# Performance work log

Measured on AMD Instinct MI355X. Metric: run time of the kernel, lower is better.

The kernel has to match this reference:

```python
import jax, jax.numpy as jnp
import numpy as np

B, WS, I, H, M_FRAC, PRE = 512, 128, 256, 512, 0.5, 24
NWS = int(WS * M_FRAC)  # 64


def setup_inputs() -> dict:
    key = jax.random.key(0)
    ks = jax.random.split(key, 9)
    s = 0.05
    return {
        "x": jax.random.normal(ks[0], (B, WS, I), dtype=jnp.float32),
        "fc1_w": jax.random.normal(ks[1], (NWS, WS), dtype=jnp.float32) * s,
        "fc1_b": jax.random.normal(ks[2], (NWS,), dtype=jnp.float32) * s,
        "W_ih": jax.random.normal(ks[3], (3 * H, I), dtype=jnp.float32) * s,
        "W_hh": jax.random.normal(ks[4], (3 * H, H), dtype=jnp.float32) * s,
        "b_ih": jax.random.normal(ks[5], (3 * H,), dtype=jnp.float32) * s,
        "b_hh": jax.random.normal(ks[6], (3 * H,), dtype=jnp.float32) * s,
        "fc2_w": jax.random.normal(ks[7], (I, H), dtype=jnp.float32) * s,
        "fc2_b": jax.random.normal(ks[8], (I,), dtype=jnp.float32) * s,
        "pre_len": PRE,
    }


def reference(x, fc1_w, fc1_b, W_ih, W_hh, b_ih, b_hh, fc2_w, fc2_b, pre_len):
    h_dim = W_hh.shape[1]
    # fc1 over the time axis: [B,WS,I] -> transpose -> [B,I,WS] -> [B,I,NWS] -> [B,NWS,I]
    y = jnp.einsum("bit,nt->bin", x.transpose(0, 2, 1), fc1_w) + fc1_b
    y = y.transpose(0, 2, 1)  # [B, NWS, I]

    # Precompute input-side gate projections for all timesteps (one big GEMM)
    gx_all = jnp.einsum("bti,gi->btg", y, W_ih) + b_ih  # [B, NWS, 3H]
    gx_all = gx_all.swapaxes(0, 1)  # time-major [NWS, B, 3H]

    h0 = jnp.zeros((y.shape[0], h_dim), dtype=x.dtype)

    def step(h, gx):
        gh = h @ W_hh.T + b_hh  # [B, 3H]
        r = jax.nn.sigmoid(gx[:, :h_dim] + gh[:, :h_dim])
        z = jax.nn.sigmoid(gx[:, h_dim:2 * h_dim] + gh[:, h_dim:2 * h_dim])
        n = jnp.tanh(gx[:, 2 * h_dim:] + r * gh[:, 2 * h_dim:])
        h_new = (1.0 - z) * n + z * h
        return h_new, h_new

    _, h_seq = jax.lax.scan(step, h0, gx_all)  # [NWS, B, H]
    h_seq = h_seq.swapaxes(0, 1)  # [B, NWS, H]
    out = jnp.einsum("bth,oh->bto", h_seq, fc2_w) + fc2_b  # [B, NWS, I]
    return out[:, -pre_len:, :]
```

## Files before the change

### kernel.cpp

```cpp
#include <hip/hip_runtime.h>
#include <math.h>

#define B_DIM 512
#define WS_DIM 128
#define I_DIM 256
#define H_DIM 512
#define NWS 64
#define PRE 24
#define SEQ0 (NWS - PRE)

typedef __attribute__((ext_vector_type(8))) short short8;
typedef __attribute__((ext_vector_type(4))) float f32x4;

#define MFMA16(a, b, c) __builtin_amdgcn_mfma_f32_16x16x32_bf16((a), (b), (c), 0, 0, 0)

__device__ __forceinline__ unsigned short f2bf(float f) {
    unsigned u = __float_as_uint(f);
    u += 0x7FFF + ((u >> 16) & 1);
    return (unsigned short)(u >> 16);
}
__device__ __forceinline__ float bf2f(unsigned short h) {
    return __uint_as_float(((unsigned)h) << 16);
}

__device__ __forceinline__ unsigned ld_dev(const unsigned* p) {
    return __hip_atomic_load((unsigned*)p, __ATOMIC_RELAXED, __HIP_MEMORY_SCOPE_AGENT);
}
__device__ __forceinline__ unsigned long long ld_dev64(const unsigned long long* p) {
    return __hip_atomic_load((unsigned long long*)p, __ATOMIC_RELAXED, __HIP_MEMORY_SCOPE_AGENT);
}
__device__ __forceinline__ void st_dev(unsigned* p, unsigned v) {
    __hip_atomic_store(p, v, __ATOMIC_RELAXED, __HIP_MEMORY_SCOPE_AGENT);
}

__global__ void __launch_bounds__(256) fc1_kernel(const float* __restrict__ x,
                                                  const float* __restrict__ fc1_w,
                                                  const float* __restrict__ fc1_b,
                                                  unsigned short* __restrict__ y) {
    __shared__ float wsm[NWS * WS_DIM];
    const int b = blockIdx.x;
    const int i = threadIdx.x;

    for (int idx = i; idx < NWS * WS_DIM; idx += 256) wsm[idx] = fc1_w[idx];
    __syncthreads();

    float acc[NWS];
#pragma unroll
    for (int n = 0; n < NWS; ++n) acc[n] = fc1_b[n];

    const float* xb = x + (size_t)b * WS_DIM * I_DIM + i;
    for (int t = 0; t < WS_DIM; ++t) {
        float xv = xb[(size_t)t * I_DIM];
#pragma unroll
        for (int n = 0; n < NWS; ++n) acc[n] += xv * wsm[n * WS_DIM + t];
    }

    unsigned short* yb = y + (size_t)b * NWS * I_DIM + i;
#pragma unroll
    for (int n = 0; n < NWS; ++n) yb[(size_t)n * I_DIM] = f2bf(acc[n]);
}

#define LDSB (24 * 96 * 64)

__global__ void __launch_bounds__(256, 1)
gru_persist(const unsigned short* __restrict__ y,
            const float* __restrict__ Wih, const float* __restrict__ bih,
            const float* __restrict__ Whh, const float* __restrict__ bhh,
            unsigned short* __restrict__ hA,
            unsigned short* __restrict__ hB,
            unsigned short* __restrict__ hseq,
            unsigned* __restrict__ flags) {
    extern __shared__ char lds[];
    const int tid = threadIdx.x;
    const int lane = tid & 63;
    const int w = tid >> 6;
    const int wm = w & 1;
    const int jh = w >> 1;
    const int bt = blockIdx.x & 15;
    const int jt = blockIdx.x >> 4;
    const int b0 = bt * 32;
    const int j0 = jt * 32;

    for (int idx = tid; idx < 96 * 768; idx += 256) {
        int n = idx / 768, k = idx % 768;
        int g = n >> 5, jj = n & 31;
        int srow = g * H_DIM + j0 + jj;
        float wv = (k < I_DIM) ? Wih[(size_t)srow * I_DIM + k]
                               : Whh[(size_t)srow * H_DIM + (k - I_DIM)];
        int ks = k >> 5, q = (k & 31) >> 3, e = k & 7;
        int byteoff = ks * 6144 + (((n * 64 + q * 16) ^ ((n & 7) << 4)) + e * 2);
        *(unsigned short*)(lds + byteoff) = f2bf(wv);
    }

    const int row16 = lane & 15;
    const int qg = lane >> 4;
    const int bbA = b0 + wm * 16 + row16;
    const int jj = jh * 16 + row16;
    const int j = j0 + jj;

    const int n0r = jj, n1r = 32 + jj, n2r = 64 + jj;
    const int bof0 = (n0r * 64 + qg * 16) ^ ((n0r & 7) << 4);
    const int bof1 = (n1r * 64 + qg * 16) ^ ((n1r & 7) << 4);
    const int bof2 = (n2r * 64 + qg * 16) ^ ((n2r & 7) << 4);

    const float br_i = bih[j], br_h = bhh[j];
    const float bz_i = bih[H_DIM + j], bz_h = bhh[H_DIM + j];
    const float bn_i = bih[2 * H_DIM + j], bn_h = bhh[2 * H_DIM + j];

    __syncthreads();

    const unsigned short* ybase = y + (size_t)bbA * NWS * I_DIM + qg * 8;

    short8 yf0[8], yf1[8];
#pragma unroll
    for (int ks = 0; ks < 8; ++ks) yf0[ks] = *(const short8*)(ybase + ks * 32);

    auto STEP = [&](int step, short8(&yc)[8], short8(&yn)[8]) {
        const unsigned short* hin = (step & 1) ? hB : hA;
        unsigned short* hout      = (step & 1) ? hA : hB;

        f32x4 aR = {br_i, br_i, br_i, br_i};
        f32x4 aZ = {bz_i, bz_i, bz_i, bz_i};
        f32x4 aN = {bn_i, bn_i, bn_i, bn_i};

#pragma unroll
        for (int ks = 0; ks < 8; ++ks) {
            short8 bf0 = *(const short8*)(lds + ks * 6144 + bof0);
            short8 bf1 = *(const short8*)(lds + ks * 6144 + bof1);
            short8 bf2 = *(const short8*)(lds + ks * 6144 + bof2);
            aR = MFMA16(yc[ks], bf0, aR);
            aZ = MFMA16(yc[ks], bf1, aZ);
            aN = MFMA16(yc[ks], bf2, aN);
        }

        int sn = (step + 1 < NWS) ? step + 1 : NWS - 1;
        const unsigned short* ypn = ybase + (size_t)sn * I_DIM;
#pragma unroll
        for (int ks = 0; ks < 8; ++ks) yn[ks] = *(const short8*)(ypn + ks * 32);

        if (step > 0) {
            const unsigned* dw = flags + ((size_t)bt * NWS + (step - 1)) * 16;
            while (true) {
                unsigned v = ld_dev(dw + (lane & 15));
                if (__all(v != 0)) break;
                __builtin_amdgcn_s_sleep(1);
            }
            asm volatile("" ::: "memory");
            __syncthreads();
        }

        const unsigned long long* hq = (const unsigned long long*)(hin + (size_t)bbA * H_DIM);
        short8 hf[16];
#pragma unroll
        for (int ks = 0; ks < 16; ++ks) {
            union { unsigned long long u[2]; short8 s; } t;
            t.u[0] = ld_dev64(hq + ks * 8 + qg * 2);
            t.u[1] = ld_dev64(hq + ks * 8 + qg * 2 + 1);
            hf[ks] = t.s;
        }
        unsigned hw[4];
        const unsigned* h32 = (const unsigned*)hin;
#pragma unroll
        for (int r = 0; r < 4; ++r) {
            int brow = b0 + wm * 16 + qg * 4 + r;
            hw[r] = ld_dev(h32 + brow * (H_DIM / 2) + (j >> 1));
        }

        f32x4 hR = {br_h, br_h, br_h, br_h};
        f32x4 hZ = {bz_h, bz_h, bz_h, bz_h};
        f32x4 hN = {bn_h, bn_h, bn_h, bn_h};
#pragma unroll
        for (int ks = 0; ks < 16; ++ks) {
            short8 bf0 = *(const short8*)(lds + (8 + ks) * 6144 + bof0);
            short8 bf1 = *(const short8*)(lds + (8 + ks) * 6144 + bof1);
            short8 bf2 = *(const short8*)(lds + (8 + ks) * 6144 + bof2);
            hR = MFMA16(hf[ks], bf0, hR);
            hZ = MFMA16(hf[ks], bf1, hZ);
            hN = MFMA16(hf[ks], bf2, hN);
        }

        unsigned short hbf[4];
#pragma unroll
        for (int r = 0; r < 4; ++r) {
            int brow = b0 + wm * 16 + qg * 4 + r;
            float pr = aR[r] + hR[r];
            float pz = aZ[r] + hZ[r];
            float rr = 1.f / (1.f + __expf(-pr));
            float zz = 1.f / (1.f + __expf(-pz));
            float pn = aN[r] + rr * hN[r];
            float ax = fabsf(pn);
            float e2 = __expf(2.f * ax);
            float nn = copysignf(1.f - 2.f / (e2 + 1.f), pn);
            float hprev = bf2f((unsigned short)((j & 1) ? (hw[r] >> 16) : (hw[r] & 0xffff)));
            float hnew = (1.f - zz) * nn + zz * hprev;
            hbf[r] = f2bf(hnew);
            unsigned v = hbf[r];
            unsigned o = __shfl_xor(v, 1);
            if (!(lane & 1))
                st_dev((unsigned*)hout + brow * (H_DIM / 2) + (j >> 1), v | (o << 16));
        }

        asm volatile("s_waitcnt vmcnt(0)" ::: "memory");
        __syncthreads();
        if (tid == 0) {
            __hip_atomic_fetch_add(flags + ((size_t)bt * NWS + step) * 16 + jt, 1u,
                                   __ATOMIC_RELAXED, __HIP_MEMORY_SCOPE_AGENT);
        }

        if (step >= SEQ0) {
#pragma unroll
            for (int r = 0; r < 4; ++r) {
                int brow = b0 + wm * 16 + qg * 4 + r;
                unsigned v = hbf[r];
                unsigned o = __shfl_xor(v, 1);
                if (!(lane & 1))
                    *(unsigned*)(hseq + ((size_t)brow * PRE + (step - SEQ0)) * H_DIM +
                                 (j & ~1)) = v | (o << 16);
            }
        }
    };

    for (int step = 0; step < NWS; step += 2) {
        STEP(step, yf0, yf1);
        STEP(step + 1, yf1, yf0);
    }
}

__global__ void __launch_bounds__(256)
fc2_mfma(const unsigned short* __restrict__ hseq,
         const unsigned short* __restrict__ w2,
         const float* __restrict__ bias,
         float* __restrict__ out) {
    const int tid = threadIdx.x;
    const int lane = tid & 63;
    const int w = tid >> 6;
    const int wm = w & 1, wn = w >> 1;
    const int row16 = lane & 15, qg = lane >> 4;
    const int mbase = blockIdx.x * 64 + wm * 32;
    const int nbase = wn * 128;

    f32x4 acc[2][8];
#pragma unroll
    for (int mt = 0; mt < 2; ++mt)
#pragma unroll
        for (int nt = 0; nt < 8; ++nt) acc[mt][nt] = f32x4{0.f, 0.f, 0.f, 0.f};

    const unsigned short* ap = hseq + (size_t)(mbase + row16) * H_DIM + qg * 8;
    const unsigned short* bp = w2 + (size_t)(nbase + row16) * H_DIM + qg * 8;
#pragma unroll
    for (int ks = 0; ks < 16; ++ks) {
        short8 a0 = *(const short8*)(ap + ks * 32);
        short8 a1 = *(const short8*)(ap + 16 * H_DIM + ks * 32);
        short8 bfr[8];
#pragma unroll
        for (int nt = 0; nt < 8; ++nt)
            bfr[nt] = *(const short8*)(bp + (size_t)nt * 16 * H_DIM + ks * 32);
#pragma unroll
        for (int nt = 0; nt < 8; ++nt) {
            acc[0][nt] = MFMA16(a0, bfr[nt], acc[0][nt]);
            acc[1][nt] = MFMA16(a1, bfr[nt], acc[1][nt]);
        }
    }

#pragma unroll
    for (int mt = 0; mt < 2; ++mt)
#pragma unroll
        for (int nt = 0; nt < 8; ++nt)
#pragma unroll
            for (int r = 0; r < 4; ++r) {
                int row = mbase + mt * 16 + qg * 4 + r;
                int col = nbase + nt * 16 + row16;
                out[(size_t)row * I_DIM + col] = acc[mt][nt][r] + bias[col];
            }
}

__global__ void cvt_w2(const float* __restrict__ w, unsigned short* __restrict__ o, int n) {
    int i = blockIdx.x * 256 + threadIdx.x;
    if (i < n) o[i] = f2bf(w[i]);
}

extern "C" void kernel_launch(void* const* d_in, const int* in_sizes, int n_in,
                              void* d_out, int out_size, void* d_ws, size_t ws_size,
                              hipStream_t stream) {
    const float* x     = (const float*)d_in[0];
    const float* fc1_w = (const float*)d_in[1];
    const float* fc1_b = (const float*)d_in[2];
    const float* W_ih  = (const float*)d_in[3];
    const float* W_hh  = (const float*)d_in[4];
    const float* b_ih  = (const float*)d_in[5];
    const float* b_hh  = (const float*)d_in[6];
    const float* fc2_w = (const float*)d_in[7];
    const float* fc2_b = (const float*)d_in[8];
    float* out = (float*)d_out;

    unsigned short* ws = (unsigned short*)d_ws;
    unsigned short* y_bf  = ws;
    unsigned short* h0    = ws + 8388608;
    unsigned short* h1    = ws + 8650752;
    unsigned short* hseq  = ws + 8912896;
    unsigned short* w2_bf = ws + 15204352;
    unsigned* flags = (unsigned*)(ws + 15335424);

    hipMemsetAsync(h0, 0, 262144 * sizeof(unsigned short), stream);
    hipMemsetAsync(flags, 0, 16 * NWS * 16 * sizeof(unsigned), stream);

    cvt_w2<<<dim3((I_DIM * H_DIM + 255) / 256), dim3(256), 0, stream>>>(
        fc2_w, w2_bf, I_DIM * H_DIM);

    fc1_kernel<<<dim3(B_DIM), dim3(256), 0, stream>>>(x, fc1_w, fc1_b, y_bf);

    hipFuncSetAttribute((const void*)gru_persist,
                        hipFuncAttributeMaxDynamicSharedMemorySize, LDSB);

    gru_persist<<<dim3(256), dim3(256), LDSB, stream>>>(
        y_bf, W_ih, b_ih, W_hh, b_hh, h0, h1, hseq, flags);

    fc2_mfma<<<dim3((B_DIM * PRE) / 64), dim3(256), 0, stream>>>(
        hseq, w2_bf, fc2_b, out);
}
```

Measured before the change: 592.0 us.

## Keep recurrent W_hh fragments in registers and carry h_prev in registers

The recurrent weight tile W_hh is now converted to bf16 once per thread and held in 48 short8 register fragments, so the per-step hidden-side MFMAs no longer read B operands from LDS. Only W_ih stays in LDS, which shrinks shared memory to a static 48 KB and drops the dynamic-LDS attribute call. The previous hidden value for the elementwise update is kept in registers across steps instead of being reloaded from global memory each step. This removes LDS traffic and a global load from the serial recurrence, at the cost of roughly 192 extra VGPRs per thread and a risk of spilling.

After: 549.6 us, median of 3. -7.2%, faster.

```diff
diff --git a/kernel.cpp b/kernel.cpp
--- a/kernel.cpp
+++ b/kernel.cpp
@@ -22,6 +22,16 @@
 __device__ __forceinline__ float bf2f(unsigned short h) {
     return __uint_as_float(((unsigned)h) << 16);
 }
+__device__ __forceinline__ short8 cvt8(const float* p) {
+    float4 lo = *(const float4*)p;
+    float4 hi = *(const float4*)(p + 4);
+    short8 r;
+    r[0] = (short)f2bf(lo.x); r[1] = (short)f2bf(lo.y);
+    r[2] = (short)f2bf(lo.z); r[3] = (short)f2bf(lo.w);
+    r[4] = (short)f2bf(hi.x); r[5] = (short)f2bf(hi.y);
+    r[6] = (short)f2bf(hi.z); r[7] = (short)f2bf(hi.w);
+    return r;
+}
 
 __device__ __forceinline__ unsigned ld_dev(const unsigned* p) {
     return __hip_atomic_load((unsigned*)p, __ATOMIC_RELAXED, __HIP_MEMORY_SCOPE_AGENT);
@@ -59,8 +69,6 @@
 #pragma unroll
     for (int n = 0; n < NWS; ++n) yb[(size_t)n * I_DIM] = f2bf(acc[n]);
 }
-
-#define LDSB (24 * 96 * 64)
 
 __global__ void __launch_bounds__(256, 1)
 gru_persist(const unsigned short* __restrict__ y,
@@ -70,7 +78,7 @@
             unsigned short* __restrict__ hB,
             unsigned short* __restrict__ hseq,
             unsigned* __restrict__ flags) {
-    extern __shared__ char lds[];
+    __shared__ char lds[8 * 6144];
     const int tid = threadIdx.x;
     const int lane = tid & 63;
     const int w = tid >> 6;
@@ -81,12 +89,10 @@
     const int b0 = bt * 32;
     const int j0 = jt * 32;
 
-    for (int idx = tid; idx < 96 * 768; idx += 256) {
-        int n = idx / 768, k = idx % 768;
-        int g = n >> 5, jj = n & 31;
-        int srow = g * H_DIM + j0 + jj;
-        float wv = (k < I_DIM) ? Wih[(size_t)srow * I_DIM + k]
-                               : Whh[(size_t)srow * H_DIM + (k - I_DIM)];
+    for (int idx = tid; idx < 96 * 256; idx += 256) {
+        int n = idx >> 8, k = idx & 255;
+        int g = n >> 5, jj2 = n & 31;
+        float wv = Wih[(size_t)(g * H_DIM + j0 + jj2) * I_DIM + k];
         int ks = k >> 5, q = (k & 31) >> 3, e = k & 7;
         int byteoff = ks * 6144 + (((n * 64 + q * 16) ^ ((n & 7) << 4)) + e * 2);
         *(unsigned short*)(lds + byteoff) = f2bf(wv);
@@ -98,6 +104,13 @@
     const int jj = jh * 16 + row16;
     const int j = j0 + jj;
 
+    short8 wh[16][3];
+#pragma unroll
+    for (int ks = 0; ks < 16; ++ks)
+#pragma unroll
+        for (int g = 0; g < 3; ++g)
+            wh[ks][g] = cvt8(&Whh[(size_t)(g * H_DIM + j0 + jj) * H_DIM + ks * 32 + qg * 8]);
+
     const int n0r = jj, n1r = 32 + jj, n2r = 64 + jj;
     const int bof0 = (n0r * 64 + qg * 16) ^ ((n0r & 7) << 4);
     const int bof1 = (n1r * 64 + qg * 16) ^ ((n1r & 7) << 4);
@@ -114,6 +127,8 @@
     short8 yf0[8], yf1[8];
 #pragma unroll
     for (int ks = 0; ks < 8; ++ks) yf0[ks] = *(const short8*)(ybase + ks * 32);
+
+    unsigned short hprevreg[4] = {0, 0, 0, 0};
 
     auto STEP = [&](int step, short8(&yc)[8], short8(&yn)[8]) {
         const unsigned short* hin = (step & 1) ? hB : hA;
@@ -158,25 +173,15 @@
             t.u[1] = ld_dev64(hq + ks * 8 + qg * 2 + 1);
             hf[ks] = t.s;
         }
-        unsigned hw[4];
-        const unsigned* h32 = (const unsigned*)hin;
-#pragma unroll
-        for (int r = 0; r < 4; ++r) {
-            int brow = b0 + wm * 16 + qg * 4 + r;
-            hw[r] = ld_dev(h32 + brow * (H_DIM / 2) + (j >> 1));
-        }
 
         f32x4 hR = {br_h, br_h, br_h, br_h};
         f32x4 hZ = {bz_h, bz_h, bz_h, bz_h};
         f32x4 hN = {bn_h, bn_h, bn_h, bn_h};
 #pragma unroll
         for (int ks = 0; ks < 16; ++ks) {
-            short8 bf0 = *(const short8*)(lds + (8 + ks) * 6144 + bof0);
-            short8 bf1 = *(const short8*)(lds + (8 + ks) * 6144 + bof1);
-            short8 bf2 = *(const short8*)(lds + (8 + ks) * 6144 + bof2);
-            hR = MFMA16(hf[ks], bf0, hR);
-            hZ = MFMA16(hf[ks], bf1, hZ);
-            hN = MFMA16(hf[ks], bf2, hN);
+            hR = MFMA16(hf[ks], wh[ks][0], hR);
+            hZ = MFMA16(hf[ks], wh[ks][1], hZ);
+            hN = MFMA16(hf[ks], wh[ks][2], hN);
         }
 
         unsigned short hbf[4];
@@ -191,9 +196,10 @@
             float ax = fabsf(pn);
             float e2 = __expf(2.f * ax);
             float nn = copysignf(1.f - 2.f / (e2 + 1.f), pn);
-            float hprev = bf2f((unsigned short)((j & 1) ? (hw[r] >> 16) : (hw[r] & 0xffff)));
+            float hprev = bf2f(hprevreg[r]);
             float hnew = (1.f - zz) * nn + zz * hprev;
             hbf[r] = f2bf(hnew);
+            hprevreg[r] = hbf[r];
             unsigned v = hbf[r];
             unsigned o = __shfl_xor(v, 1);
             if (!(lane & 1))
@@ -309,10 +315,7 @@
 
     fc1_kernel<<<dim3(B_DIM), dim3(256), 0, stream>>>(x, fc1_w, fc1_b, y_bf);
 
-    hipFuncSetAttribute((const void*)gru_persist,
-                        hipFuncAttributeMaxDynamicSharedMemorySize, LDSB);
-
-    gru_persist<<<dim3(256), dim3(256), LDSB, stream>>>(
+    gru_persist<<<dim3(256), dim3(256), 0, stream>>>(
         y_bf, W_ih, b_ih, W_hh, b_hh, h0, h1, hseq, flags);
 
     fc2_mfma<<<dim3((B_DIM * PRE) / 64), dim3(256), 0, stream>>>(
```
